# Optimization experiments

Hardware: AMD Instinct MI355X
Metric: run time of the kernel (lower is better)

## Reference

```python
import jax, jax.numpy as jnp
import numpy as np

MARGIN = 0.2
BETA = 0.8333333
EPS = 1e-8          # torch cosine_similarity eps
BIG = 1.0e9         # sentinel used by the torch code for masking

B, M, FEAT, RES = 64, 2048, 512, 32


def setup_inputs() -> dict:
    key = jax.random.key(0)
    k1, k2, k3, k4 = jax.random.split(key, 4)
    return {
        "anchor_features": jax.random.normal(k1, (B, FEAT), dtype=jnp.float32),
        "true_voxels": jax.random.uniform(k2, (B, RES, RES, RES), dtype=jnp.float32),
        "memory_keys": jax.random.normal(k3, (M, FEAT), dtype=jnp.float32),
        "memory_values": jax.random.uniform(k4, (M, RES, RES, RES), dtype=jnp.float32),
    }


def reference(anchor_features, true_voxels, memory_keys, memory_values):
    b = true_voxels.shape[0]
    m = memory_values.shape[0]
    v = true_voxels.reshape(b, -1)        # (B, N) with N = res^3
    w = memory_values.reshape(m, -1)      # (M, N)
    n = v.shape[1]

    # Pairwise voxel MSE via ||a||^2 - 2ab + ||b||^2 GEMM trick (same math,
    # avoids the (B, M, N) broadcast intermediate).
    v_sq = jnp.sum(v * v, axis=1)                         # (B,)
    w_sq = jnp.sum(w * w, axis=1)                         # (M,)
    mse = (v_sq[:, None] + w_sq[None, :] - 2.0 * (v @ w.T)) / n   # (B, M)
    sv_scores = 1.0 - mse

    pos_mask = sv_scores > BETA
    neg_mask = sv_scores < BETA

    # Pairwise cosine distance 1 - cos_sim (norms clamped at eps like torch).
    a_norm = jnp.maximum(jnp.linalg.norm(anchor_features, axis=1, keepdims=True), EPS)
    k_norm = jnp.maximum(jnp.linalg.norm(memory_keys, axis=1, keepdims=True), EPS)
    key_dists = 1.0 - (anchor_features / a_norm) @ (memory_keys / k_norm).T  # (B, M)

    hardest_pos = jnp.max(jnp.where(pos_mask, key_dists, -BIG), axis=1)  # (B,)
    hardest_neg = jnp.min(jnp.where(neg_mask, key_dists, BIG), axis=1)   # (B,)

    loss = jnp.maximum(hardest_pos - hardest_neg + MARGIN, 0.0)          # (B,)

    valid = jnp.any(pos_mask, axis=1) & jnp.any(neg_mask, axis=1)        # (B,)
    cnt = jnp.sum(valid.astype(loss.dtype))
    total = jnp.sum(jnp.where(valid, loss, 0.0))
    # Masked mean; 0.0 when no valid triplets (mirrors the torch early-return).
    return jnp.where(cnt > 0, total / jnp.maximum(cnt, 1.0), 0.0)
```

## Files before the change

### kernel.cpp

```cpp
#include <hip/hip_runtime.h>


typedef __attribute__((ext_vector_type(8)))  short bf16x8;
typedef __attribute__((ext_vector_type(16))) float f32x16;

constexpr int   Mdim   = 2048;
constexpr int   Nvox   = 32768;
constexpr int   NS     = 16;
constexpr float BETA   = 0.8333333f;
constexpr float MARGIN = 0.2f;
constexpr float BIGV   = 1.0e9f;

constexpr size_t OFF_VSQP = 0;
constexpr size_t OFF_AINV = 1024;
constexpr size_t OFF_KINV = 1088;
constexpr size_t OFF_WSQ  = 3136;
constexpr size_t OFF_WSQP = 5184;
constexpr size_t OFF_PHP  = 37952;
constexpr size_t OFF_PHN  = 38208;
constexpr size_t OFF_PAP  = 38464;
constexpr size_t OFF_PAN  = 38720;
constexpr size_t OFF_KEYP = 38976;
constexpr size_t OFF_DOTP = 170048;
constexpr size_t OFF_VHI  = 2267200;
constexpr size_t OFF_VLO  = 3315776;

__device__ __forceinline__ unsigned int bf16rne(float x) {
    unsigned int u = __float_as_uint(x);
    return (u + 0x7FFFu + ((u >> 16) & 1u)) >> 16;
}
__device__ __forceinline__ int pk2(unsigned int lo, unsigned int hi) {
    return (int)(lo | (hi << 16));
}
__device__ __forceinline__ void async16(const ushort* g, ushort* l) {
    __builtin_amdgcn_global_load_lds(
        (const __attribute__((address_space(1))) unsigned int*)g,
        (__attribute__((address_space(3))) unsigned int*)l, 16, 0, 0);
}

__global__ __launch_bounds__(256) void prep_kernel(
    const float* __restrict__ vox, const float* __restrict__ anc,
    const float* __restrict__ keys,
    ushort* __restrict__ vhi, ushort* __restrict__ vlo,
    float* __restrict__ vsqp, float* __restrict__ ainv, float* __restrict__ kinv)
{
    const int tid = threadIdx.x;
    if (blockIdx.x < 256) {
        const int bg = blockIdx.x >> 4;
        const int ks = blockIdx.x & 15;
        const int bsub = tid & 3;
        const int b  = bg * 4 + bsub;
        const int kw = tid >> 2;
        float sq = 0.f;
        #pragma unroll
        for (int it = 0; it < 2; ++it) {
            const int kloc = ks * 2048 + (it * 64 + kw) * 16;
            const float4* src = reinterpret_cast<const float4*>(vox + (size_t)b * Nvox + kloc);
            float4 x[4];
            #pragma unroll
            for (int j = 0; j < 4; ++j) x[j] = src[j];
            unsigned int h[16], l[16];
            #pragma unroll
            for (int j = 0; j < 4; ++j) {
                const float e[4] = {x[j].x, x[j].y, x[j].z, x[j].w};
                #pragma unroll
                for (int q = 0; q < 4; ++q) {
                    const float v = e[q];
                    sq = fmaf(v, v, sq);
                    const unsigned int hb = bf16rne(v);
                    h[j*4+q] = hb;
                    const float r = v - __uint_as_float(hb << 16);
                    l[j*4+q] = bf16rne(r);
                }
            }
            const int c = kloc >> 6, s = (kloc >> 4) & 3;
            const size_t base = (size_t)c * 4096 + (b >> 5) * 2048 + s * 512 + (b & 31) * 8;
            int4 hp0 = { pk2(h[0],h[1]), pk2(h[2],h[3]), pk2(h[4],h[5]), pk2(h[6],h[7]) };
            int4 hp1 = { pk2(h[8],h[9]), pk2(h[10],h[11]), pk2(h[12],h[13]), pk2(h[14],h[15]) };
            int4 lp0 = { pk2(l[0],l[1]), pk2(l[2],l[3]), pk2(l[4],l[5]), pk2(l[6],l[7]) };
            int4 lp1 = { pk2(l[8],l[9]), pk2(l[10],l[11]), pk2(l[12],l[13]), pk2(l[14],l[15]) };
            *reinterpret_cast<int4*>(vhi + base)       = hp0;
            *reinterpret_cast<int4*>(vhi + base + 256) = hp1;
            *reinterpret_cast<int4*>(vlo + base)       = lp0;
            *reinterpret_cast<int4*>(vlo + base + 256) = lp1;
        }
        #pragma unroll
        for (int off = 32; off >= 4; off >>= 1) sq += __shfl_down(sq, off);
        __shared__ float red[16];
        const int lane = tid & 63, wave = tid >> 6;
        if (lane < 4) red[wave * 4 + lane] = sq;
        __syncthreads();
        if (tid < 4)
            vsqp[(size_t)(bg * 4 + tid) * 16 + ks] =
                red[tid] + red[tid + 4] + red[tid + 8] + red[tid + 12];
    } else {
        const int r = (blockIdx.x - 256) * 4 + (tid >> 6);
        const int lane = tid & 63;
        const float* src = (r < 64) ? (anc + (size_t)r * 512)
                                    : (keys + (size_t)(r - 64) * 512);
        const float4* s4 = reinterpret_cast<const float4*>(src);
        float4 x = s4[lane];
        float4 y = s4[lane + 64];
        float p = 0.f;
        p = fmaf(x.x, x.x, p); p = fmaf(x.y, x.y, p);
        p = fmaf(x.z, x.z, p); p = fmaf(x.w, x.w, p);
        p = fmaf(y.x, y.x, p); p = fmaf(y.y, y.y, p);
        p = fmaf(y.z, y.z, p); p = fmaf(y.w, y.w, p);
        #pragma unroll
        for (int off = 32; off > 0; off >>= 1) p += __shfl_down(p, off);
        if (lane == 0) {
            float inv = 1.f / fmaxf(sqrtf(p), 1e-8f);
            if (r < 64) ainv[r] = inv; else kinv[r - 64] = inv;
        }
    }
}

__global__ __launch_bounds__(256) void gemm_big(
    const ushort* __restrict__ vhi, const ushort* __restrict__ vlo,
    const float* __restrict__ W,
    float* __restrict__ dotp, float* __restrict__ wsqp)
{
    __shared__ ushort sVhi[4096], sVlo[4096], sWhi[4096];
    __shared__ float red[256];

    const int tid  = threadIdx.x;
    const int lane = tid & 63;
    const int wave = tid >> 6;
    const int mb   = blockIdx.x & 31;
    const int ns   = blockIdx.x >> 5;
    const int srow = tid >> 2;
    const int sq   = tid & 3;

    const float*  wptr = W + (size_t)(mb * 64 + srow) * Nvox + ns * 2048 + sq * 16;
    const ushort* vhig = vhi + (size_t)(ns * 32) * 4096 + wave * 1024 + lane * 8;
    const ushort* vlog = vlo + (size_t)(ns * 32) * 4096 + wave * 1024 + lane * 8;
    ushort* ldsVhi = &sVhi[wave * 1024];
    ushort* ldsVlo = &sVlo[wave * 1024];

    const int wr = wave >> 1, wc = wave & 1;
    f32x16 acc = {};
    float wsq = 0.f;

    float4 wreg[4];
    #pragma unroll
    for (int j = 0; j < 4; ++j) wreg[j] = *reinterpret_cast<const float4*>(wptr + j * 4);

    const int woff0 = (srow >> 5) * 2048 + sq * 512 + (srow & 31) * 8;

    for (int ch = 0; ch < 32; ++ch) {
        int4 p0, p1;
        {
            unsigned int hb[16];
            #pragma unroll
            for (int j = 0; j < 4; ++j) {
                const float e[4] = {wreg[j].x, wreg[j].y, wreg[j].z, wreg[j].w};
                #pragma unroll
                for (int q = 0; q < 4; ++q) {
                    wsq = fmaf(e[q], e[q], wsq);
                    hb[j*4+q] = bf16rne(e[q]);
                }
            }
            p0 = (int4){ pk2(hb[0],hb[1]), pk2(hb[2],hb[3]), pk2(hb[4],hb[5]), pk2(hb[6],hb[7]) };
            p1 = (int4){ pk2(hb[8],hb[9]), pk2(hb[10],hb[11]), pk2(hb[12],hb[13]), pk2(hb[14],hb[15]) };
        }
        __syncthreads();
        async16(vhig + (size_t)ch * 4096,       ldsVhi);
        async16(vhig + (size_t)ch * 4096 + 512, ldsVhi + 512);
        async16(vlog + (size_t)ch * 4096,       ldsVlo);
        async16(vlog + (size_t)ch * 4096 + 512, ldsVlo + 512);
        *reinterpret_cast<int4*>(&sWhi[woff0])       = p0;
        *reinterpret_cast<int4*>(&sWhi[woff0 + 256]) = p1;
        if (ch < 31) {
            #pragma unroll
            for (int j = 0; j < 4; ++j)
                wreg[j] = *reinterpret_cast<const float4*>(wptr + (ch + 1) * 64 + j * 4);
        }
        __syncthreads();
        #pragma unroll
        for (int s = 0; s < 4; ++s) {
            bf16x8 ah = *reinterpret_cast<const bf16x8*>(&sVhi[wr * 2048 + s * 512 + lane * 8]);
            bf16x8 al = *reinterpret_cast<const bf16x8*>(&sVlo[wr * 2048 + s * 512 + lane * 8]);
            bf16x8 bh = *reinterpret_cast<const bf16x8*>(&sWhi[wc * 2048 + s * 512 + lane * 8]);
            acc = __builtin_amdgcn_mfma_f32_32x32x16_bf16(ah, bh, acc, 0, 0, 0);
            acc = __builtin_amdgcn_mfma_f32_32x32x16_bf16(al, bh, acc, 0, 0, 0);
        }
    }

    const int col   = lane & 31;
    const int rbase = 4 * (lane >> 5);
    const size_t out_m = (size_t)(mb * 64 + wc * 32 + col);
    #pragma unroll
    for (int r = 0; r < 16; ++r) {
        const int row = (r & 3) + 8 * (r >> 2) + rbase;
        const int b   = wr * 32 + row;
        dotp[(size_t)(ns * 64 + b) * Mdim + out_m] = acc[r];
    }
    red[tid] = wsq;
    __syncthreads();
    if (tid < 64)
        wsqp[(size_t)ns * Mdim + mb * 64 + tid] =
            red[tid*4] + red[tid*4+1] + red[tid*4+2] + red[tid*4+3];
}

__global__ __launch_bounds__(256) void keydist_kernel(
    const float* __restrict__ anc, const float* __restrict__ keys,
    const float* __restrict__ wsqp, float* __restrict__ keyp,
    float* __restrict__ wsq)
{
    const int tid = threadIdx.x;
    if (blockIdx.x >= 256) {
        const int m = (blockIdx.x - 256) * 256 + tid;
        float s = 0.f;
        #pragma unroll
        for (int sp = 0; sp < NS; ++sp) s += wsqp[(size_t)sp * Mdim + m];
        wsq[m] = s;
        return;
    }
    __shared__ float kk[8 * 516];
    const int mt = blockIdx.x * 8;
    {
        const int row = tid >> 5, colb = (tid & 31) * 16;
        const float4* src = reinterpret_cast<const float4*>(keys + (size_t)(mt + row) * 512 + colb);
        #pragma unroll
        for (int j = 0; j < 4; ++j)
            *reinterpret_cast<float4*>(&kk[row * 516 + colb + j * 4]) = src[j];
    }
    __syncthreads();
    const int b = tid >> 2, msub = tid & 3;
    const float* arow = anc + (size_t)b * 512;
    const float* k0 = &kk[msub * 516];
    const float* k1 = &kk[(msub + 4) * 516];
    float d0 = 0.f, d1 = 0.f;
    for (int k = 0; k < 512; k += 4) {
        const float4 a = *reinterpret_cast<const float4*>(arow + k);
        const float4 x = *reinterpret_cast<const float4*>(k0 + k);
        const float4 y = *reinterpret_cast<const float4*>(k1 + k);
        d0 = fmaf(a.x, x.x, d0); d0 = fmaf(a.y, x.y, d0);
        d0 = fmaf(a.z, x.z, d0); d0 = fmaf(a.w, x.w, d0);
        d1 = fmaf(a.x, y.x, d1); d1 = fmaf(a.y, y.y, d1);
        d1 = fmaf(a.z, y.z, d1); d1 = fmaf(a.w, y.w, d1);
    }
    keyp[(size_t)b * Mdim + mt + msub]     = d0;
    keyp[(size_t)b * Mdim + mt + msub + 4] = d1;
}

__global__ __launch_bounds__(256) void rowpart_kernel(
    const float* __restrict__ dotp, const float* __restrict__ wsq,
    const float* __restrict__ keyp, const float* __restrict__ vsqp,
    const float* __restrict__ ainv, const float* __restrict__ kinv,
    float* __restrict__ php, float* __restrict__ phn,
    float* __restrict__ pap, float* __restrict__ pan)
{
    const int bid = blockIdx.x, tid = threadIdx.x;
    const int b = bid >> 2, sl = bid & 3;
    float vs = 0.f;
    #pragma unroll
    for (int i = 0; i < 16; ++i) vs += vsqp[(size_t)b * 16 + i];
    const float ai = ainv[b];
    float hp = -BIGV, hn = BIGV, ap = 0.f, an = 0.f;
    #pragma unroll
    for (int rep = 0; rep < 2; ++rep) {
        const int m = sl * 512 + rep * 256 + tid;
        float dot = 0.f;
        #pragma unroll
        for (int s = 0; s < NS; ++s) dot += dotp[(size_t)(s * 64 + b) * Mdim + m];
        const float sv = 1.f - (vs + wsq[m] - 2.f * dot) * (1.f / 32768.f);
        const float kd = 1.f - keyp[(size_t)b * Mdim + m] * ai * kinv[m];
        if (sv > BETA) { ap = 1.f; hp = fmaxf(hp, kd); }
        if (sv < BETA) { an = 1.f; hn = fminf(hn, kd); }
    }
    #pragma unroll
    for (int off = 32; off > 0; off >>= 1) {
        hp = fmaxf(hp, __shfl_down(hp, off));
        hn = fminf(hn, __shfl_down(hn, off));
        ap = fmaxf(ap, __shfl_down(ap, off));
        an = fmaxf(an, __shfl_down(an, off));
    }
    __shared__ float sb[16];
    const int wv = tid >> 6;
    if ((tid & 63) == 0) {
        sb[wv * 4 + 0] = hp; sb[wv * 4 + 1] = hn;
        sb[wv * 4 + 2] = ap; sb[wv * 4 + 3] = an;
    }
    __syncthreads();
    if (tid == 0) {
        for (int w2 = 1; w2 < 4; ++w2) {
            hp = fmaxf(hp, sb[w2 * 4 + 0]);
            hn = fminf(hn, sb[w2 * 4 + 1]);
            ap = fmaxf(ap, sb[w2 * 4 + 2]);
            an = fmaxf(an, sb[w2 * 4 + 3]);
        }
        php[bid] = hp; phn[bid] = hn; pap[bid] = ap; pan[bid] = an;
    }
}

__global__ void final_kernel(const float* __restrict__ php, const float* __restrict__ phn,
                             const float* __restrict__ pap, const float* __restrict__ pan,
                             float* __restrict__ out)
{
    const int t = threadIdx.x;
    float hp = php[t], hn = phn[t], ap = pap[t], an = pan[t];
    hp = fmaxf(hp, __shfl_down(hp, 2)); hp = fmaxf(hp, __shfl_down(hp, 1));
    hn = fminf(hn, __shfl_down(hn, 2)); hn = fminf(hn, __shfl_down(hn, 1));
    ap = fmaxf(ap, __shfl_down(ap, 2)); ap = fmaxf(ap, __shfl_down(ap, 1));
    an = fmaxf(an, __shfl_down(an, 2)); an = fmaxf(an, __shfl_down(an, 1));
    __shared__ float sl[64], sc[64];
    if ((t & 3) == 0) {
        const int b = t >> 2;
        const float valid = (ap > 0.f && an > 0.f) ? 1.f : 0.f;
        sl[b] = fmaxf(hp - hn + MARGIN, 0.f) * valid;
        sc[b] = valid;
    }
    __syncthreads();
    if (t < 64) {
        float l = sl[t], c = sc[t];
        #pragma unroll
        for (int off = 32; off > 0; off >>= 1) {
            l += __shfl_down(l, off);
            c += __shfl_down(c, off);
        }
        if (t == 0) out[0] = (c > 0.f) ? (l / c) : 0.f;
    }
}

extern "C" void kernel_launch(void* const* d_in, const int* in_sizes, int n_in,
                              void* d_out, int out_size, void* d_ws, size_t ws_size,
                              hipStream_t stream) {
    const float* anchor = (const float*)d_in[0];
    const float* voxels = (const float*)d_in[1];
    const float* keys   = (const float*)d_in[2];
    const float* vals   = (const float*)d_in[3];

    float* ws = (float*)d_ws;
    float*  vsqp = ws + OFF_VSQP;
    float*  ainv = ws + OFF_AINV;
    float*  kinv = ws + OFF_KINV;
    float*  wsq  = ws + OFF_WSQ;
    float*  wsqp = ws + OFF_WSQP;
    float*  php  = ws + OFF_PHP;
    float*  phn  = ws + OFF_PHN;
    float*  pap  = ws + OFF_PAP;
    float*  pan  = ws + OFF_PAN;
    float*  keyp = ws + OFF_KEYP;
    float*  dotp = ws + OFF_DOTP;
    ushort* vhi  = (ushort*)(ws + OFF_VHI);
    ushort* vlo  = (ushort*)(ws + OFF_VLO);

    prep_kernel<<<784, 256, 0, stream>>>(voxels, anchor, keys, vhi, vlo, vsqp, ainv, kinv);
    gemm_big<<<32 * NS, 256, 0, stream>>>(vhi, vlo, vals, dotp, wsqp);
    keydist_kernel<<<264, 256, 0, stream>>>(anchor, keys, wsqp, keyp, wsq);
    rowpart_kernel<<<256, 256, 0, stream>>>(dotp, wsq, keyp, vsqp, ainv, kinv,
                                            php, phn, pap, pan);
    final_kernel<<<1, 256, 0, stream>>>(php, phn, pap, pan, (float*)d_out);
}
```

Before: 413.3 us.

## Double split-K factor in voxel GEMM and restructure prep for coalesced writes

Raises the K-split of the big voxel GEMM from 16 to 32 slices, doubling the block count to 1024 so the grid covers the GPU more fully, and adds an occupancy hint of 4 blocks per CU. The W load pattern now reads strided float4 pieces interleaved across threads, and the LDS layout for W is rewritten to match. The prep kernel now has each wave write contiguous bf16 hi/lo tiles, and it computes voxel squared norms in separate per-row blocks instead of partial sums, which simplifies rowpart. The trade-off is twice as many dotp partials to write and reduce in rowpart, plus a larger workspace.

```diff
diff --git a/kernel.cpp b/kernel.cpp
--- a/kernel.cpp
+++ b/kernel.cpp
@@ -6,24 +6,24 @@
 
 constexpr int   Mdim   = 2048;
 constexpr int   Nvox   = 32768;
-constexpr int   NS     = 16;
+constexpr int   NS     = 32;
 constexpr float BETA   = 0.8333333f;
 constexpr float MARGIN = 0.2f;
 constexpr float BIGV   = 1.0e9f;
 
-constexpr size_t OFF_VSQP = 0;
-constexpr size_t OFF_AINV = 1024;
-constexpr size_t OFF_KINV = 1088;
-constexpr size_t OFF_WSQ  = 3136;
-constexpr size_t OFF_WSQP = 5184;
-constexpr size_t OFF_PHP  = 37952;
-constexpr size_t OFF_PHN  = 38208;
-constexpr size_t OFF_PAP  = 38464;
-constexpr size_t OFF_PAN  = 38720;
-constexpr size_t OFF_KEYP = 38976;
-constexpr size_t OFF_DOTP = 170048;
-constexpr size_t OFF_VHI  = 2267200;
-constexpr size_t OFF_VLO  = 3315776;
+constexpr size_t OFF_VSQ  = 0;
+constexpr size_t OFF_AINV = 64;
+constexpr size_t OFF_KINV = 128;
+constexpr size_t OFF_WSQ  = 2176;
+constexpr size_t OFF_WSQP = 4224;
+constexpr size_t OFF_PHP  = 69760;
+constexpr size_t OFF_PHN  = 70016;
+constexpr size_t OFF_PAP  = 70272;
+constexpr size_t OFF_PAN  = 70528;
+constexpr size_t OFF_KEYP = 70784;
+constexpr size_t OFF_DOTP = 201856;
+constexpr size_t OFF_VHI  = 4396160;
+constexpr size_t OFF_VLO  = 5444736;
 
 __device__ __forceinline__ unsigned int bf16rne(float x) {
     unsigned int u = __float_as_uint(x);
@@ -42,65 +42,56 @@
     const float* __restrict__ vox, const float* __restrict__ anc,
     const float* __restrict__ keys,
     ushort* __restrict__ vhi, ushort* __restrict__ vlo,
-    float* __restrict__ vsqp, float* __restrict__ ainv, float* __restrict__ kinv)
+    float* __restrict__ vsq, float* __restrict__ ainv, float* __restrict__ kinv)
 {
     const int tid = threadIdx.x;
-    if (blockIdx.x < 256) {
-        const int bg = blockIdx.x >> 4;
-        const int ks = blockIdx.x & 15;
-        const int bsub = tid & 3;
-        const int b  = bg * 4 + bsub;
-        const int kw = tid >> 2;
-        float sq = 0.f;
-        #pragma unroll
-        for (int it = 0; it < 2; ++it) {
-            const int kloc = ks * 2048 + (it * 64 + kw) * 16;
-            const float4* src = reinterpret_cast<const float4*>(vox + (size_t)b * Nvox + kloc);
-            float4 x[4];
+    const int lane = tid & 63;
+    const int wave = tid >> 6;
+    if (blockIdx.x < 512) {
+        #pragma unroll
+        for (int u = 0; u < 2; ++u) {
+            const int uid = blockIdx.x * 8 + wave * 2 + u;
+            const int bh = uid & 1, s = (uid >> 1) & 3, c = uid >> 3;
+            const int b   = bh * 32 + (lane & 31);
+            const int col = c * 64 + s * 16 + (lane >> 5) * 8;
+            const float4* src = reinterpret_cast<const float4*>(vox + (size_t)b * Nvox + col);
+            const float4 x0 = src[0], x1 = src[1];
+            const float e[8] = {x0.x, x0.y, x0.z, x0.w, x1.x, x1.y, x1.z, x1.w};
+            unsigned int h[8], l8[8];
             #pragma unroll
-            for (int j = 0; j < 4; ++j) x[j] = src[j];
-            unsigned int h[16], l[16];
-            #pragma unroll
-            for (int j = 0; j < 4; ++j) {
-                const float e[4] = {x[j].x, x[j].y, x[j].z, x[j].w};
-                #pragma unroll
-                for (int q = 0; q < 4; ++q) {
-                    const float v = e[q];
-                    sq = fmaf(v, v, sq);
-                    const unsigned int hb = bf16rne(v);
-                    h[j*4+q] = hb;
-                    const float r = v - __uint_as_float(hb << 16);
-                    l[j*4+q] = bf16rne(r);
-                }
+            for (int q = 0; q < 8; ++q) {
+                const unsigned int hb = bf16rne(e[q]);
+                h[q] = hb;
+                l8[q] = bf16rne(e[q] - __uint_as_float(hb << 16));
             }
-            const int c = kloc >> 6, s = (kloc >> 4) & 3;
-            const size_t base = (size_t)c * 4096 + (b >> 5) * 2048 + s * 512 + (b & 31) * 8;
-            int4 hp0 = { pk2(h[0],h[1]), pk2(h[2],h[3]), pk2(h[4],h[5]), pk2(h[6],h[7]) };
-            int4 hp1 = { pk2(h[8],h[9]), pk2(h[10],h[11]), pk2(h[12],h[13]), pk2(h[14],h[15]) };
-            int4 lp0 = { pk2(l[0],l[1]), pk2(l[2],l[3]), pk2(l[4],l[5]), pk2(l[6],l[7]) };
-            int4 lp1 = { pk2(l[8],l[9]), pk2(l[10],l[11]), pk2(l[12],l[13]), pk2(l[14],l[15]) };
-            *reinterpret_cast<int4*>(vhi + base)       = hp0;
-            *reinterpret_cast<int4*>(vhi + base + 256) = hp1;
-            *reinterpret_cast<int4*>(vlo + base)       = lp0;
-            *reinterpret_cast<int4*>(vlo + base + 256) = lp1;
-        }
-        #pragma unroll
-        for (int off = 32; off >= 4; off >>= 1) sq += __shfl_down(sq, off);
-        __shared__ float red[16];
-        const int lane = tid & 63, wave = tid >> 6;
-        if (lane < 4) red[wave * 4 + lane] = sq;
+            const int4 hp = { pk2(h[0],h[1]), pk2(h[2],h[3]), pk2(h[4],h[5]), pk2(h[6],h[7]) };
+            const int4 lp = { pk2(l8[0],l8[1]), pk2(l8[2],l8[3]), pk2(l8[4],l8[5]), pk2(l8[6],l8[7]) };
+            const size_t base = (size_t)c * 4096 + bh * 2048 + s * 512 + lane * 8;
+            *reinterpret_cast<int4*>(vhi + base) = hp;
+            *reinterpret_cast<int4*>(vlo + base) = lp;
+        }
+    } else if (blockIdx.x < 576) {
+        const int b = blockIdx.x - 512;
+        const float4* src = reinterpret_cast<const float4*>(vox + (size_t)b * Nvox);
+        float p = 0.f;
+        for (int i = tid; i < Nvox / 4; i += 256) {
+            const float4 x = src[i];
+            p = fmaf(x.x, x.x, p); p = fmaf(x.y, x.y, p);
+            p = fmaf(x.z, x.z, p); p = fmaf(x.w, x.w, p);
+        }
+        #pragma unroll
+        for (int off = 32; off > 0; off >>= 1) p += __shfl_down(p, off);
+        __shared__ float sb[4];
+        if (lane == 0) sb[wave] = p;
         __syncthreads();
-        if (tid < 4)
-            vsqp[(size_t)(bg * 4 + tid) * 16 + ks] =
-                red[tid] + red[tid + 4] + red[tid + 8] + red[tid + 12];
+        if (tid == 0) vsq[b] = sb[0] + sb[1] + sb[2] + sb[3];
     } else {
-        const int r = (blockIdx.x - 256) * 4 + (tid >> 6);
-        const int lane = tid & 63;
+        const int r = (blockIdx.x - 576) * 4 + wave;
         const float* src = (r < 64) ? (anc + (size_t)r * 512)
                                     : (keys + (size_t)(r - 64) * 512);
         const float4* s4 = reinterpret_cast<const float4*>(src);
-        float4 x = s4[lane];
-        float4 y = s4[lane + 64];
+        const float4 x = s4[lane];
+        const float4 y = s4[lane + 64];
         float p = 0.f;
         p = fmaf(x.x, x.x, p); p = fmaf(x.y, x.y, p);
         p = fmaf(x.z, x.z, p); p = fmaf(x.w, x.w, p);
@@ -109,18 +100,18 @@
         #pragma unroll
         for (int off = 32; off > 0; off >>= 1) p += __shfl_down(p, off);
         if (lane == 0) {
-            float inv = 1.f / fmaxf(sqrtf(p), 1e-8f);
+            const float inv = 1.f / fmaxf(sqrtf(p), 1e-8f);
             if (r < 64) ainv[r] = inv; else kinv[r - 64] = inv;
         }
     }
 }
 
-__global__ __launch_bounds__(256) void gemm_big(
+__global__ __launch_bounds__(256, 4) void gemm_big(
     const ushort* __restrict__ vhi, const ushort* __restrict__ vlo,
     const float* __restrict__ W,
     float* __restrict__ dotp, float* __restrict__ wsqp)
 {
-    __shared__ ushort sVhi[4096], sVlo[4096], sWhi[4096];
+    __shared__ ushort sVhi[4096], sVlo[4096], sW[4096];
     __shared__ float red[256];
 
     const int tid  = threadIdx.x;
@@ -131,9 +122,9 @@
     const int srow = tid >> 2;
     const int sq   = tid & 3;
 
-    const float*  wptr = W + (size_t)(mb * 64 + srow) * Nvox + ns * 2048 + sq * 16;
-    const ushort* vhig = vhi + (size_t)(ns * 32) * 4096 + wave * 1024 + lane * 8;
-    const ushort* vlog = vlo + (size_t)(ns * 32) * 4096 + wave * 1024 + lane * 8;
+    const float*  wptr = W + (size_t)(mb * 64 + srow) * Nvox + ns * 1024 + sq * 4;
+    const ushort* vhig = vhi + (size_t)(ns * 16) * 4096 + wave * 1024 + lane * 8;
+    const ushort* vlog = vlo + (size_t)(ns * 16) * 4096 + wave * 1024 + lane * 8;
     ushort* ldsVhi = &sVhi[wave * 1024];
     ushort* ldsVlo = &sVlo[wave * 1024];
 
@@ -143,44 +134,42 @@
 
     float4 wreg[4];
     #pragma unroll
-    for (int j = 0; j < 4; ++j) wreg[j] = *reinterpret_cast<const float4*>(wptr + j * 4);
-
-    const int woff0 = (srow >> 5) * 2048 + sq * 512 + (srow & 31) * 8;
-
-    for (int ch = 0; ch < 32; ++ch) {
-        int4 p0, p1;
-        {
-            unsigned int hb[16];
+    for (int j = 0; j < 4; ++j) wreg[j] = *reinterpret_cast<const float4*>(wptr + j * 16);
+
+    const int woffbase = (srow >> 5) * 2048 + ((srow & 31) + 32 * (sq >> 1)) * 8 + (sq & 1) * 4;
+
+    for (int ch = 0; ch < 16; ++ch) {
+        int2 pj[4];
+        #pragma unroll
+        for (int j = 0; j < 4; ++j) {
+            const float e[4] = {wreg[j].x, wreg[j].y, wreg[j].z, wreg[j].w};
+            unsigned int hb[4];
             #pragma unroll
-            for (int j = 0; j < 4; ++j) {
-                const float e[4] = {wreg[j].x, wreg[j].y, wreg[j].z, wreg[j].w};
-                #pragma unroll
-                for (int q = 0; q < 4; ++q) {
-                    wsq = fmaf(e[q], e[q], wsq);
-                    hb[j*4+q] = bf16rne(e[q]);
-                }
+            for (int q = 0; q < 4; ++q) {
+                wsq = fmaf(e[q], e[q], wsq);
+                hb[q] = bf16rne(e[q]);
             }
-            p0 = (int4){ pk2(hb[0],hb[1]), pk2(hb[2],hb[3]), pk2(hb[4],hb[5]), pk2(hb[6],hb[7]) };
-            p1 = (int4){ pk2(hb[8],hb[9]), pk2(hb[10],hb[11]), pk2(hb[12],hb[13]), pk2(hb[14],hb[15]) };
+            pj[j] = (int2){ pk2(hb[0], hb[1]), pk2(hb[2], hb[3]) };
         }
         __syncthreads();
         async16(vhig + (size_t)ch * 4096,       ldsVhi);
         async16(vhig + (size_t)ch * 4096 + 512, ldsVhi + 512);
         async16(vlog + (size_t)ch * 4096,       ldsVlo);
         async16(vlog + (size_t)ch * 4096 + 512, ldsVlo + 512);
-        *reinterpret_cast<int4*>(&sWhi[woff0])       = p0;
-        *reinterpret_cast<int4*>(&sWhi[woff0 + 256]) = p1;
-        if (ch < 31) {
+        #pragma unroll
+        for (int j = 0; j < 4; ++j)
+            *reinterpret_cast<int2*>(&sW[woffbase + j * 512]) = pj[j];
+        if (ch < 15) {
             #pragma unroll
             for (int j = 0; j < 4; ++j)
-                wreg[j] = *reinterpret_cast<const float4*>(wptr + (ch + 1) * 64 + j * 4);
+                wreg[j] = *reinterpret_cast<const float4*>(wptr + (ch + 1) * 64 + j * 16);
         }
         __syncthreads();
         #pragma unroll
         for (int s = 0; s < 4; ++s) {
-            bf16x8 ah = *reinterpret_cast<const bf16x8*>(&sVhi[wr * 2048 + s * 512 + lane * 8]);
-            bf16x8 al = *reinterpret_cast<const bf16x8*>(&sVlo[wr * 2048 + s * 512 + lane * 8]);
-            bf16x8 bh = *reinterpret_cast<const bf16x8*>(&sWhi[wc * 2048 + s * 512 + lane * 8]);
+            const bf16x8 ah = *reinterpret_cast<const bf16x8*>(&sVhi[wr * 2048 + s * 512 + lane * 8]);
+            const bf16x8 al = *reinterpret_cast<const bf16x8*>(&sVlo[wr * 2048 + s * 512 + lane * 8]);
+            const bf16x8 bh = *reinterpret_cast<const bf16x8*>(&sW[wc * 2048 + s * 512 + lane * 8]);
             acc = __builtin_amdgcn_mfma_f32_32x32x16_bf16(ah, bh, acc, 0, 0, 0);
             acc = __builtin_amdgcn_mfma_f32_32x32x16_bf16(al, bh, acc, 0, 0, 0);
         }
@@ -246,16 +235,14 @@
 
 __global__ __launch_bounds__(256) void rowpart_kernel(
     const float* __restrict__ dotp, const float* __restrict__ wsq,
-    const float* __restrict__ keyp, const float* __restrict__ vsqp,
+    const float* __restrict__ keyp, const float* __restrict__ vsq,
     const float* __restrict__ ainv, const float* __restrict__ kinv,
     float* __restrict__ php, float* __restrict__ phn,
     float* __restrict__ pap, float* __restrict__ pan)
 {
     const int bid = blockIdx.x, tid = threadIdx.x;
     const int b = bid >> 2, sl = bid & 3;
-    float vs = 0.f;
-    #pragma unroll
-    for (int i = 0; i < 16; ++i) vs += vsqp[(size_t)b * 16 + i];
+    const float vs = vsq[b];
     const float ai = ainv[b];
     float hp = -BIGV, hn = BIGV, ap = 0.f, an = 0.f;
     #pragma unroll
@@ -332,7 +319,7 @@
     const float* vals   = (const float*)d_in[3];
 
     float* ws = (float*)d_ws;
-    float*  vsqp = ws + OFF_VSQP;
+    float*  vsq  = ws + OFF_VSQ;
     float*  ainv = ws + OFF_AINV;
     float*  kinv = ws + OFF_KINV;
     float*  wsq  = ws + OFF_WSQ;
@@ -346,10 +333,10 @@
     ushort* vhi  = (ushort*)(ws + OFF_VHI);
     ushort* vlo  = (ushort*)(ws + OFF_VLO);
 
-    prep_kernel<<<784, 256, 0, stream>>>(voxels, anchor, keys, vhi, vlo, vsqp, ainv, kinv);
+    prep_kernel<<<1104, 256, 0, stream>>>(voxels, anchor, keys, vhi, vlo, vsq, ainv, kinv);
     gemm_big<<<32 * NS, 256, 0, stream>>>(vhi, vlo, vals, dotp, wsqp);
     keydist_kernel<<<264, 256, 0, stream>>>(anchor, keys, wsqp, keyp, wsq);
-    rowpart_kernel<<<256, 256, 0, stream>>>(dotp, wsq, keyp, vsqp, ainv, kinv,
+    rowpart_kernel<<<256, 256, 0, stream>>>(dotp, wsq, keyp, vsq, ainv, kinv,
                                             php, phn, pap, pan);
     final_kernel<<<1, 256, 0, stream>>>(php, phn, pap, pan, (float*)d_out);
 }
```

Measured after the change: 423.7 us. 2.5% more time.
